# Performance work log

Hardware: AMD Instinct MI355X
Metric: run time of the kernel (lower is better)

## Reference

```python
import jax, jax.numpy as jnp
import numpy as np

NBITS = 2
Q_T = 1
Q_ALPHA = 0.9
NORM_PPF_0_75 = 0.6745
IN_FEATURES = 4096
OUT_FEATURES = 4096
TOKENS = 8192

# signed bit encodings: rows of {-1,+1}^NBITS for codes 0..2^NBITS-1
_bitvecs = np.unpackbits(np.arange(2 ** NBITS, dtype=np.uint8).reshape(-1, 1), axis=1)[:, -NBITS:]
ENCODINGS = jnp.asarray(_bitvecs.astype(np.float32) * 2.0 - 1.0)  # [2^nbits, nbits]


def setup_inputs() -> dict:
    key = jax.random.key(0)
    k1, k2, k3 = jax.random.split(key, 3)
    m, n = IN_FEATURES, OUT_FEATURES
    x = jax.random.normal(k1, (TOKENS, m), dtype=jnp.float32)
    # matches linear.weight.data.normal_(0, sqrt(2/(m+n)))
    weight = jax.random.normal(k2, (n, m), dtype=jnp.float32) * np.sqrt(2.0 / (m + n))
    bias = jax.random.normal(k3, (n,), dtype=jnp.float32) * 0.01
    base = NORM_PPF_0_75 * (2.0 / n) ** 0.5 / 2 ** (NBITS - 1)
    basis = jnp.asarray([base * 2.0 ** i for i in range(NBITS)], dtype=jnp.float32)
    return {"x": x, "weight": weight, "bias": bias, "basis": basis}


def _quantize(w, basis, encodings):
    # qlevels[k] = <encodings[k], basis>, then sort levels ascending
    qlevels = encodings @ basis                      # [2^nbits]
    order = jnp.argsort(qlevels)
    qlevels = qlevels[order]
    enc = encodings[order]                           # [2^nbits, nbits]
    # midpoints between adjacent levels; bucketize replaces the per-level mask loop:
    # level i iff  thres[i-1] < w <= thres[i]  (w <= thres[0] -> 0, w > thres[-1] -> last)
    thres = 0.5 * (qlevels[:-1] + qlevels[1:])       # [2^nbits - 1]
    idx = jnp.searchsorted(thres, w.ravel(), side="left")  # [N]
    wq = qlevels[idx].reshape(w.shape)               # quantized weights
    wb = enc[idx]                                    # [N, nbits] signed codes
    return wq, wb


def reference(x, weight, bias, basis):
    # training-mode learned quantization: quantize, then least-squares basis refit
    v = basis
    w_flat = weight.ravel()
    for _ in range(Q_T):
        wq, wb = _quantize(weight, v, ENCODINGS)
        # solve (wb^T wb) v = wb^T w   (nbits x nbits system)
        v = jnp.linalg.solve(wb.T @ wb, wb.T @ w_flat)
    new_basis = Q_ALPHA * basis + (1.0 - Q_ALPHA) * v
    # straight-through estimator: forward uses wq, backward passes grad to weight
    wq_ste = weight + jax.lax.stop_gradient(wq - weight)
    out = x @ wq_ste.T + bias                        # [tokens, out_features]
    del new_basis  # buffer update; not part of the forward output tensor
    return out
```

## Files before the change

kernel.cpp:

```cpp
#include <hip/hip_runtime.h>
#include <hip/hip_bf16.h>


#define M_TOK 8192
#define N_OUT 4096
#define K_IN  4096

typedef __attribute__((ext_vector_type(8))) short short8;
typedef __attribute__((ext_vector_type(4))) float floatx4;

typedef __attribute__((address_space(1))) const void gvoid_t;
typedef __attribute__((address_space(3))) void lvoid_t;

__device__ __forceinline__ ushort f2bf(float f) {
    unsigned u = __float_as_uint(f);
    u += 0x7fffu + ((u >> 16) & 1u);
    return (ushort)(u >> 16);
}

#define PREP_XBLK 2048
#define PREP_WBLK 1024

__global__ __launch_bounds__(256) void prep(
        const float4* __restrict__ x,  short8* __restrict__ xb,
        const float4* __restrict__ w,  const float* __restrict__ basis,
        short8* __restrict__ wqo) {
    if (blockIdx.x < PREP_XBLK) {
        const int tid    = blockIdx.x * 256 + threadIdx.x;
        const int stride = PREP_XBLK * 256;
        const int n8     = (M_TOK * K_IN) / 8;
        for (int i = tid; i < n8; i += stride) {
            float4 a = x[2 * i], b = x[2 * i + 1];
            short8 o;
            o[0] = (short)f2bf(a.x); o[1] = (short)f2bf(a.y);
            o[2] = (short)f2bf(a.z); o[3] = (short)f2bf(a.w);
            o[4] = (short)f2bf(b.x); o[5] = (short)f2bf(b.y);
            o[6] = (short)f2bf(b.z); o[7] = (short)f2bf(b.w);
            xb[i] = o;
        }
    } else {
        float b0 = basis[0], b1 = basis[1];
        float l0 = -b0 - b1, l1 = -b0 + b1, l2 = b0 - b1, l3 = b0 + b1;
        float t;
        if (l0 > l1) { t = l0; l0 = l1; l1 = t; }
        if (l2 > l3) { t = l2; l2 = l3; l3 = t; }
        if (l0 > l2) { t = l0; l0 = l2; l2 = t; }
        if (l1 > l3) { t = l1; l1 = l3; l3 = t; }
        if (l1 > l2) { t = l1; l1 = l2; l2 = t; }
        const float t0 = 0.5f * (l0 + l1), t1 = 0.5f * (l1 + l2), t2 = 0.5f * (l2 + l3);
        const int tid    = (blockIdx.x - PREP_XBLK) * 256 + threadIdx.x;
        const int stride = PREP_WBLK * 256;
        const int n8     = (N_OUT * K_IN) / 8;
#define QF(vv) ((vv > t1) ? ((vv > t2) ? l3 : l2) : ((vv > t0) ? l1 : l0))
        for (int i = tid; i < n8; i += stride) {
            float4 a = w[2 * i], b = w[2 * i + 1];
            short8 o;
            o[0] = (short)f2bf(QF(a.x)); o[1] = (short)f2bf(QF(a.y));
            o[2] = (short)f2bf(QF(a.z)); o[3] = (short)f2bf(QF(a.w));
            o[4] = (short)f2bf(QF(b.x)); o[5] = (short)f2bf(QF(b.y));
            o[6] = (short)f2bf(QF(b.z)); o[7] = (short)f2bf(QF(b.w));
            wqo[i] = o;
        }
#undef QF
    }
}


#define NIT 32

#define BAR() do { asm volatile("" ::: "memory"); \
                   __builtin_amdgcn_s_barrier(); \
                   asm volatile("" ::: "memory"); \
                   __builtin_amdgcn_sched_barrier(0); } while (0)
#define VMC6() asm volatile("s_waitcnt vmcnt(6)" ::: "memory")
#define VMC0() asm volatile("s_waitcnt vmcnt(0)" ::: "memory")

#define STAGE_A(tt, h) do { const int _p = (tt) & 1;                          \
    __builtin_amdgcn_global_load_lds(                                         \
        (gvoid_t*)(ag + (size_t)((h) * 128) * K_IN + (tt) * 64),              \
        (lvoid_t*)(As + _p * 16384 + ((h) * 128 + wid * 16) * 64), 16, 0, 0); \
    __builtin_amdgcn_global_load_lds(                                         \
        (gvoid_t*)(ag + (size_t)((h) * 128 + 8) * K_IN + (tt) * 64),          \
        (lvoid_t*)(As + _p * 16384 + ((h) * 128 + wid * 16 + 8) * 64), 16, 0, 0); \
} while (0)
#define STAGE_B(tt, h) do { const int _p = (tt) & 1;                          \
    __builtin_amdgcn_global_load_lds(                                         \
        (gvoid_t*)(bg + (size_t)((h) * 128) * K_IN + (tt) * 64),              \
        (lvoid_t*)(Bs + _p * 16384 + ((h) * 128 + wid * 16) * 64), 16, 0, 0); \
    __builtin_amdgcn_global_load_lds(                                         \
        (gvoid_t*)(bg + (size_t)((h) * 128 + 8) * K_IN + (tt) * 64),          \
        (lvoid_t*)(Bs + _p * 16384 + ((h) * 128 + wid * 16 + 8) * 64), 16, 0, 0); \
} while (0)

#define MFMA_PAIR(MA, MB) do {                                                \
    __builtin_amdgcn_s_setprio(1);                                           \
    _Pragma("unroll") for (int nj = 0; nj < 4; ++nj) {                        \
        acc[MA][nj] = __builtin_amdgcn_mfma_f32_16x16x32_bf16(                \
            af[MA][0], bfv[nj][0], acc[MA][nj], 0, 0, 0);                     \
        acc[MA][nj] = __builtin_amdgcn_mfma_f32_16x16x32_bf16(                \
            af[MA][1], bfv[nj][1], acc[MA][nj], 0, 0, 0);                     \
    }                                                                         \
    _Pragma("unroll") for (int nj = 0; nj < 4; ++nj) {                        \
        acc[MB][nj] = __builtin_amdgcn_mfma_f32_16x16x32_bf16(                \
            af[MB][0], bfv[nj][0], acc[MB][nj], 0, 0, 0);                     \
        acc[MB][nj] = __builtin_amdgcn_mfma_f32_16x16x32_bf16(                \
            af[MB][1], bfv[nj][1], acc[MB][nj], 0, 0, 0);                     \
    }                                                                         \
    __builtin_amdgcn_s_setprio(0);                                            \
} while (0)

#define GROUP4(PB, TS1, C1, TS2, CM) do {                                     \
    const ushort* Ab = As + (PB) * 16384;                                     \
    const ushort* Bb = Bs + (PB) * 16384;                                     \
    short8 af[8][2], bfv[4][2];                                               \
                            \
    _Pragma("unroll") for (int nj = 0; nj < 4; ++nj)                          \
        _Pragma("unroll") for (int ks = 0; ks < 2; ++ks)                      \
            bfv[nj][ks] = *(const short8*)(Bb + (wn + nj * 16 + mrow) * 64 + (cswz ^ (ks * 32))); \
    _Pragma("unroll") for (int mi = 0; mi < 2; ++mi)                          \
        _Pragma("unroll") for (int ks = 0; ks < 2; ++ks)                      \
            af[mi][ks] = *(const short8*)(Ab + (wm + mi * 16 + mrow) * 64 + (cswz ^ (ks * 32))); \
    if (C1) { STAGE_A(TS1, 1); }                                              \
    BAR();                                                                    \
    MFMA_PAIR(0, 1);                                                          \
    BAR();                                                                    \
                                    \
    _Pragma("unroll") for (int mi = 2; mi < 6; ++mi)                          \
        _Pragma("unroll") for (int ks = 0; ks < 2; ++ks)                      \
            af[mi][ks] = *(const short8*)(Ab + (wm + mi * 16 + mrow) * 64 + (cswz ^ (ks * 32))); \
    if (CM) { STAGE_B(TS2, 0); }                                              \
    BAR();                                                                    \
    MFMA_PAIR(2, 3);                                                          \
    BAR();                                                                    \
                                   \
    _Pragma("unroll") for (int mi = 6; mi < 8; ++mi)                          \
        _Pragma("unroll") for (int ks = 0; ks < 2; ++ks)                      \
            af[mi][ks] = *(const short8*)(Ab + (wm + mi * 16 + mrow) * 64 + (cswz ^ (ks * 32))); \
    if (CM) { STAGE_B(TS2, 1); }                                              \
    BAR();                                                                    \
    MFMA_PAIR(4, 5);                                                          \
    BAR();                                                                    \
                                                       \
    if (CM) { STAGE_A(TS2, 0); VMC6(); } else { VMC0(); }                     \
    BAR();                                                                    \
    MFMA_PAIR(6, 7);                                                          \
    BAR();                                                                    \
} while (0)

extern "C" __global__ __launch_bounds__(512, 2) void gemm256(
        const ushort* __restrict__ A,
        const ushort* __restrict__ B,
        const float* __restrict__ bias,
        float* __restrict__ C) {
    extern __shared__ ushort smem[];
    ushort* As = smem;
    ushort* Bs = smem + 32768;

    const int tid  = threadIdx.x;
    const int lane = tid & 63;
    const int wid  = tid >> 6;
    const int wr   = wid >> 2;
    const int wc   = wid & 3;
    const int wm   = wr * 128;
    const int wn   = wc * 64;

    const int bid = blockIdx.x;
    const int swz = (bid & 7) * 64 + (bid >> 3);
    const int bn0 = (swz & 15) * 256;
    const int bm0 = (swz >> 4) * 256;

    const int lr = lane >> 3, lc = lane & 7;
    const ushort* ag = A + (size_t)(bm0 + wid * 16 + lr) * K_IN + (lc ^ lr) * 8;
    const ushort* bg = B + (size_t)(bn0 + wid * 16 + lr) * K_IN + (lc ^ lr) * 8;

    const int mrow = lane & 15;
    const int quad = lane >> 4;
    const int cswz = (quad ^ (mrow & 7)) * 8;

    floatx4 acc[8][4] = {};

    STAGE_B(0, 0); STAGE_B(0, 1); STAGE_A(0, 0); STAGE_A(0, 1);
    STAGE_B(1, 0); STAGE_B(1, 1); STAGE_A(1, 0);
    VMC6();
    BAR();

#pragma unroll 1
    for (int it = 0; it < NIT; ++it) {
        const bool more = (it + 1 < NIT);
        GROUP4(0, 2 * it + 1, true, 2 * it + 2, more);
        GROUP4(1, 2 * it + 2, more, 2 * it + 3, more);
    }

    const int r0 = (lane >> 4) * 4;
    const int cc = lane & 15;
#pragma unroll
    for (int nj = 0; nj < 4; ++nj) {
        const int col = bn0 + wn + nj * 16 + cc;
        const float bj = bias[col];
#pragma unroll
        for (int mi = 0; mi < 8; ++mi) {
#pragma unroll
            for (int r = 0; r < 4; ++r) {
                const int row = bm0 + wm + mi * 16 + r0 + r;
                C[(size_t)row * N_OUT + col] = acc[mi][nj][r] + bj;
            }
        }
    }
}

extern "C" void kernel_launch(void* const* d_in, const int* in_sizes, int n_in,
                              void* d_out, int out_size, void* d_ws, size_t ws_size,
                              hipStream_t stream) {
    const float* x     = (const float*)d_in[0];
    const float* w     = (const float*)d_in[1];
    const float* bias  = (const float*)d_in[2];
    const float* basis = (const float*)d_in[3];
    float* out = (float*)d_out;

    ushort* Xb = (ushort*)d_ws;
    ushort* Wq = Xb + (size_t)M_TOK * K_IN;

    prep<<<PREP_XBLK + PREP_WBLK, 256, 0, stream>>>(
        (const float4*)x, (short8*)Xb, (const float4*)w, basis, (short8*)Wq);

    (void)hipFuncSetAttribute((const void*)gemm256,
                              hipFuncAttributeMaxDynamicSharedMemorySize, 131072);
    gemm256<<<dim3(512), 512, 131072, stream>>>(Xb, Wq, bias, out);
}
```

Measured before the change: 490.2 us.

## Switch GEMM inner loop to 32x32x16 bf16 MFMA with fewer LDS reads

Replaces the 16x16x32 MFMA tiling (8x4 fragments per wave) with 32x32x16 MFMA (4x2 fragments), changing the LDS read pattern, the swizzle offsets and the epilogue row mapping to match. Each phase now issues 8 larger MFMAs per k-step, and fewer LDS fragment reads are needed per FLOP. It also drops the sched_barrier from the barrier macro, which gives the compiler more freedom to interleave instructions. The risk is that the swizzle or output mapping is wrong, and that the different register pressure or instruction schedule changes overlap.

```diff
diff --git a/kernel.cpp b/kernel.cpp
--- a/kernel.cpp
+++ b/kernel.cpp
@@ -7,7 +7,7 @@
 #define K_IN  4096
 
 typedef __attribute__((ext_vector_type(8))) short short8;
-typedef __attribute__((ext_vector_type(4))) float floatx4;
+typedef __attribute__((ext_vector_type(16))) float floatx16;
 
 typedef __attribute__((address_space(1))) const void gvoid_t;
 typedef __attribute__((address_space(3))) void lvoid_t;
@@ -68,10 +68,9 @@
 
 #define NIT 32
 
-#define BAR() do { asm volatile("" ::: "memory"); \
-                   __builtin_amdgcn_s_barrier(); \
-                   asm volatile("" ::: "memory"); \
-                   __builtin_amdgcn_sched_barrier(0); } while (0)
+#define BARm() do { asm volatile("" ::: "memory"); \
+                    __builtin_amdgcn_s_barrier(); \
+                    asm volatile("" ::: "memory"); } while (0)
 #define VMC6() asm volatile("s_waitcnt vmcnt(6)" ::: "memory")
 #define VMC0() asm volatile("s_waitcnt vmcnt(0)" ::: "memory")
 
@@ -92,59 +91,54 @@
         (lvoid_t*)(Bs + _p * 16384 + ((h) * 128 + wid * 16 + 8) * 64), 16, 0, 0); \
 } while (0)
 
-#define MFMA_PAIR(MA, MB) do {                                                \
-    __builtin_amdgcn_s_setprio(1);                                           \
-    _Pragma("unroll") for (int nj = 0; nj < 4; ++nj) {                        \
-        acc[MA][nj] = __builtin_amdgcn_mfma_f32_16x16x32_bf16(                \
-            af[MA][0], bfv[nj][0], acc[MA][nj], 0, 0, 0);                     \
-        acc[MA][nj] = __builtin_amdgcn_mfma_f32_16x16x32_bf16(                \
-            af[MA][1], bfv[nj][1], acc[MA][nj], 0, 0, 0);                     \
-    }                                                                         \
-    _Pragma("unroll") for (int nj = 0; nj < 4; ++nj) {                        \
-        acc[MB][nj] = __builtin_amdgcn_mfma_f32_16x16x32_bf16(                \
-            af[MB][0], bfv[nj][0], acc[MB][nj], 0, 0, 0);                     \
-        acc[MB][nj] = __builtin_amdgcn_mfma_f32_16x16x32_bf16(                \
-            af[MB][1], bfv[nj][1], acc[MB][nj], 0, 0, 0);                     \
+#define READ_A(FI) do {                                                       \
+    _Pragma("unroll") for (int s = 0; s < 4; ++s)                             \
+        av[s] = *(const short8*)(Ab + (FI) * 2048 + csz[s]);                  \
+} while (0)
+
+#define MFMA_PH(FI) do {                                                      \
+    __builtin_amdgcn_s_setprio(1);                                            \
+    _Pragma("unroll") for (int s = 0; s < 4; ++s) {                           \
+        acc[FI][0] = __builtin_amdgcn_mfma_f32_32x32x16_bf16(                 \
+            av[s], bf[0][s], acc[FI][0], 0, 0, 0);                            \
+        acc[FI][1] = __builtin_amdgcn_mfma_f32_32x32x16_bf16(                 \
+            av[s], bf[1][s], acc[FI][1], 0, 0, 0);                            \
     }                                                                         \
     __builtin_amdgcn_s_setprio(0);                                            \
 } while (0)
 
 #define GROUP4(PB, TS1, C1, TS2, CM) do {                                     \
-    const ushort* Ab = As + (PB) * 16384;                                     \
-    const ushort* Bb = Bs + (PB) * 16384;                                     \
-    short8 af[8][2], bfv[4][2];                                               \
+    const ushort* Ab = As + (PB) * 16384 + (wm + mrow32) * 64;                \
+    const ushort* Bb = Bs + (PB) * 16384 + (wn + mrow32) * 64;                \
+    short8 av[4], bf[2][4];                                                   \
                             \
-    _Pragma("unroll") for (int nj = 0; nj < 4; ++nj)                          \
-        _Pragma("unroll") for (int ks = 0; ks < 2; ++ks)                      \
-            bfv[nj][ks] = *(const short8*)(Bb + (wn + nj * 16 + mrow) * 64 + (cswz ^ (ks * 32))); \
-    _Pragma("unroll") for (int mi = 0; mi < 2; ++mi)                          \
-        _Pragma("unroll") for (int ks = 0; ks < 2; ++ks)                      \
-            af[mi][ks] = *(const short8*)(Ab + (wm + mi * 16 + mrow) * 64 + (cswz ^ (ks * 32))); \
+    _Pragma("unroll") for (int s = 0; s < 4; ++s) {                           \
+        bf[0][s] = *(const short8*)(Bb + csz[s]);                             \
+        bf[1][s] = *(const short8*)(Bb + 2048 + csz[s]);                      \
+    }                                                                         \
+    READ_A(0);                                                                \
     if (C1) { STAGE_A(TS1, 1); }                                              \
-    BAR();                                                                    \
-    MFMA_PAIR(0, 1);                                                          \
-    BAR();                                                                    \
-                                    \
-    _Pragma("unroll") for (int mi = 2; mi < 6; ++mi)                          \
-        _Pragma("unroll") for (int ks = 0; ks < 2; ++ks)                      \
-            af[mi][ks] = *(const short8*)(Ab + (wm + mi * 16 + mrow) * 64 + (cswz ^ (ks * 32))); \
+    BARm();                                                                   \
+    MFMA_PH(0);                                                               \
+    BARm();                                                                   \
+                                                        \
+    READ_A(1);                                                                \
     if (CM) { STAGE_B(TS2, 0); }                                              \
-    BAR();                                                                    \
-    MFMA_PAIR(2, 3);                                                          \
-    BAR();                                                                    \
-                                   \
-    _Pragma("unroll") for (int mi = 6; mi < 8; ++mi)                          \
-        _Pragma("unroll") for (int ks = 0; ks < 2; ++ks)                      \
-            af[mi][ks] = *(const short8*)(Ab + (wm + mi * 16 + mrow) * 64 + (cswz ^ (ks * 32))); \
+    BARm();                                                                   \
+    MFMA_PH(1);                                                               \
+    BARm();                                                                   \
+                                                        \
+    READ_A(2);                                                                \
     if (CM) { STAGE_B(TS2, 1); }                                              \
-    BAR();                                                                    \
-    MFMA_PAIR(4, 5);                                                          \
-    BAR();                                                                    \
-                                                       \
+    BARm();                                                                   \
+    MFMA_PH(2);                                                               \
+    BARm();                                                                   \
+                                                        \
+    READ_A(3);                                                                \
     if (CM) { STAGE_A(TS2, 0); VMC6(); } else { VMC0(); }                     \
-    BAR();                                                                    \
-    MFMA_PAIR(6, 7);                                                          \
-    BAR();                                                                    \
+    BARm();                                                                   \
+    MFMA_PH(3);                                                               \
+    BARm();                                                                   \
 } while (0)
 
 extern "C" __global__ __launch_bounds__(512, 2) void gemm256(
@@ -173,16 +167,19 @@
     const ushort* ag = A + (size_t)(bm0 + wid * 16 + lr) * K_IN + (lc ^ lr) * 8;
     const ushort* bg = B + (size_t)(bn0 + wid * 16 + lr) * K_IN + (lc ^ lr) * 8;
 
-    const int mrow = lane & 15;
-    const int quad = lane >> 4;
-    const int cswz = (quad ^ (mrow & 7)) * 8;
-
-    floatx4 acc[8][4] = {};
+    const int mrow32 = lane & 31;
+    const int half   = lane >> 5;
+    int csz[4];
+#pragma unroll
+    for (int s = 0; s < 4; ++s)
+        csz[s] = (((2 * s) | half) ^ (mrow32 & 7)) * 8;
+
+    floatx16 acc[4][2] = {};
 
     STAGE_B(0, 0); STAGE_B(0, 1); STAGE_A(0, 0); STAGE_A(0, 1);
     STAGE_B(1, 0); STAGE_B(1, 1); STAGE_A(1, 0);
     VMC6();
-    BAR();
+    BARm();
 
 #pragma unroll 1
     for (int it = 0; it < NIT; ++it) {
@@ -191,17 +188,16 @@
         GROUP4(1, 2 * it + 2, more, 2 * it + 3, more);
     }
 
-    const int r0 = (lane >> 4) * 4;
-    const int cc = lane & 15;
-#pragma unroll
-    for (int nj = 0; nj < 4; ++nj) {
-        const int col = bn0 + wn + nj * 16 + cc;
+    const int cc = lane & 31;
+#pragma unroll
+    for (int nj = 0; nj < 2; ++nj) {
+        const int col = bn0 + wn + nj * 32 + cc;
         const float bj = bias[col];
 #pragma unroll
-        for (int mi = 0; mi < 8; ++mi) {
-#pragma unroll
-            for (int r = 0; r < 4; ++r) {
-                const int row = bm0 + wm + mi * 16 + r0 + r;
+        for (int mi = 0; mi < 4; ++mi) {
+#pragma unroll
+            for (int r = 0; r < 16; ++r) {
+                const int row = bm0 + wm + mi * 32 + (r & 3) + 8 * (r >> 2) + 4 * half;
                 C[(size_t)row * N_OUT + col] = acc[mi][nj][r] + bj;
             }
         }
```

Measured after the change: 494.9 us. Within noise of the previous version (+1.0%).
